# Kernel optimization log

Measured on AMD Instinct MI355X. Metric: run time of the kernel, lower is better.

Reference implementation:

```python
import jax, jax.numpy as jnp
import numpy as np


def setup_inputs() -> dict:
    key = jax.random.key(0)
    ks = jax.random.split(key, 5)
    B, T, I, H = 64, 512, 512, 512
    s_i = 1.0 / np.sqrt(H)
    return {
        "x": jax.random.normal(ks[0], (B, T, I), dtype=jnp.float32),
        "w_ih": jax.random.normal(ks[1], (4 * H, I), dtype=jnp.float32) * s_i,
        "w_hh": jax.random.normal(ks[2], (4 * H, H), dtype=jnp.float32) * s_i,
        "b_ih": jax.random.normal(ks[3], (4 * H,), dtype=jnp.float32) * s_i,
        "b_hh": jax.random.normal(ks[4], (4 * H,), dtype=jnp.float32) * s_i,
    }


def reference(x, w_ih, w_hh, b_ih, b_hh):
    # x: [B, T, I] (batch_first). Torch permutes to [T, B, I] then loops LSTMCell.
    B, T, I = x.shape
    H = w_hh.shape[1]
    # Precompute input contribution to gates for all timesteps: [T, B, 4H]
    x_gates = jnp.einsum('bti,gi->tbg', x, w_ih) + b_ih + b_hh
    h0 = jnp.zeros((B, H), dtype=x.dtype)  # hidden_init='zero'
    c0 = jnp.zeros((B, H), dtype=x.dtype)

    def step(carry, xg_t):
        h, c = carry
        gates = xg_t + h @ w_hh.T  # [B, 4H]
        i, f, g, o = jnp.split(gates, 4, axis=-1)  # torch LSTMCell order i,f,g,o
        i = jax.nn.sigmoid(i)
        f = jax.nn.sigmoid(f)
        g = jnp.tanh(g)
        o = jax.nn.sigmoid(o)
        c = f * c + i * g
        h = o * jnp.tanh(c)
        return (h, c), h

    (_, _), hs = jax.lax.scan(step, (h0, c0), x_gates)
    # return_sequences=True: torch stacks along dim 0 -> [T, B, H]
    return hs
```

## Files before the change

### kernel.cpp

```cpp
#include <hip/hip_runtime.h>
#include <stdint.h>


#define BATCH 64
#define TSTEPS 512
#define IDIM 512
#define HDIM 512
#define NGROUPS 8
#define BB 8
#define NWG (NGROUPS * 32)
#define HDAT_U64 (BB * (HDIM / 2))

typedef __attribute__((ext_vector_type(4))) float f32x4;
typedef __attribute__((ext_vector_type(8))) short bf16x8;
typedef __attribute__((ext_vector_type(4))) unsigned int u32x4;
typedef __attribute__((ext_vector_type(2))) unsigned int u32x2;

#define AS(p, v) __hip_atomic_store((p), (v), __ATOMIC_RELAXED, __HIP_MEMORY_SCOPE_AGENT)

__device__ inline unsigned short f2bf(float f) {
  unsigned u = __builtin_bit_cast(unsigned, f);
  u = (u + 0x7fffu + ((u >> 16) & 1u)) >> 16;
  return (unsigned short)u;
}
__device__ inline float fast_sigmoid(float x) { return 1.f / (1.f + __expf(-x)); }
__device__ inline float fast_tanh(float x) { return 1.f - 2.f / (__expf(2.f * x) + 1.f); }

__global__ void lstm_init(const float* __restrict__ b_ih, const float* __restrict__ b_hh,
                          float* __restrict__ bias, uint64_t* __restrict__ hdat) {
  const int i = blockIdx.x * blockDim.x + threadIdx.x;
  if (i < 4 * HDIM) bias[i] = b_ih[i] + b_hh[i];
  for (int j = i; j < 2 * NGROUPS * HDAT_U64; j += 2048) hdat[j] = 0ull;
}

__global__ __launch_bounds__(256, 1)
void lstm_persistent(const float* __restrict__ x,
                     const float* __restrict__ w_ih,
                     const float* __restrict__ w_hh,
                     const float* __restrict__ bias,
                     uint64_t* hdat,
                     float* __restrict__ out) {
  __shared__ unsigned short X_lds[2][8 * IDIM];
  __shared__ unsigned short H_lds[2][8 * HDIM];

  const int wg = blockIdx.x;
  const int group = wg >> 5;
  const int rank = wg & 31;
  const int b0 = group * BB;
  const int h0 = rank * 16;
  const int tid = threadIdx.x;
  const int wave = tid >> 6;
  const int lane = tid & 63;
  const int hi4 = lane >> 4;
  const int nn = lane & 15;

  const int growf = (nn & 3) * HDIM + h0 + wave * 4 + (nn >> 2);
  bf16x8 breg[32];
#pragma unroll
  for (int kt = 0; kt < 32; ++kt) {
    const int k = kt * 32 + hi4 * 8;
    const float* src = (k < IDIM) ? (w_ih + (size_t)growf * IDIM + k)
                                  : (w_hh + (size_t)growf * HDIM + (k - IDIM));
    bf16x8 v;
#pragma unroll
    for (int j = 0; j < 8; ++j) v[j] = (short)f2bf(src[j]);
    breg[kt] = v;
  }
  const int mycol = h0 + wave * 4 + hi4;
  const float bv0 = bias[0 * HDIM + mycol];
  const float bv1 = bias[1 * HDIM + mycol];
  const float bv2 = bias[2 * HDIM + mycol];
  const float bv3 = bias[3 * HDIM + mycol];

  const int bi = lane & 15;
  const int mr8 = bi & 7;
  const int rswz = mr8 << 4;

#pragma unroll
  for (int q = 0; q < 2; ++q) {
    const int r = wave + q * 4;
    const float* xp = x + ((size_t)(b0 + r) * TSTEPS + 0) * IDIM + lane * 8;
    float4 fa = *(const float4*)xp;
    float4 fb = *(const float4*)(xp + 4);
    bf16x8 v;
    v[0] = (short)f2bf(fa.x); v[1] = (short)f2bf(fa.y);
    v[2] = (short)f2bf(fa.z); v[3] = (short)f2bf(fa.w);
    v[4] = (short)f2bf(fb.x); v[5] = (short)f2bf(fb.y);
    v[6] = (short)f2bf(fb.z); v[7] = (short)f2bf(fb.w);
    *(bf16x8*)((char*)&X_lds[0][0] + ((r * 1024 + lane * 16) ^ ((r & 7) << 4))) = v;
  }
  float4 xfA[4], xfB[4];
#pragma unroll
  for (int q = 0; q < 2; ++q) {
    const float* xp = x + ((size_t)(b0 + wave + q * 4) * TSTEPS + 1) * IDIM + lane * 8;
    xfA[q * 2] = *(const float4*)xp;
    xfA[q * 2 + 1] = *(const float4*)(xp + 4);
  }
  __syncthreads();

  float c = 0.f;
  float hout[8];
  const size_t obase = (size_t)(b0 + bi) * HDIM + mycol;

  for (int tb = 0; tb < TSTEPS; tb += 8) {
#pragma unroll
    for (int u = 0; u < 8; ++u) {
      const int t = tb + u;
      const int cur = t & 1;
      const uint32_t tu = (uint32_t)t;

      f32x4 acc0 = {0.f, 0.f, 0.f, 0.f}, acc1 = {0.f, 0.f, 0.f, 0.f};
#pragma unroll
      for (int kt = 0; kt < 16; kt += 2) {
        bf16x8 a0 = *(const bf16x8*)((const char*)&X_lds[cur][0] +
                      ((mr8 * 1024 + (kt * 4 + hi4) * 16) ^ rswz));
        acc0 = __builtin_amdgcn_mfma_f32_16x16x32_bf16(breg[kt], a0, acc0, 0, 0, 0);
        bf16x8 a1 = *(const bf16x8*)((const char*)&X_lds[cur][0] +
                      ((mr8 * 1024 + ((kt + 1) * 4 + hi4) * 16) ^ rswz));
        acc1 = __builtin_amdgcn_mfma_f32_16x16x32_bf16(breg[kt + 1], a1, acc1, 0, 0, 0);
      }

      if (t > 0) {
        const uint64_t* dp = hdat + ((size_t)cur * NGROUPS + group) * HDAT_U64
                           + (size_t)wave * 512 + lane * 2;
        u32x4 d0, d1, d2, d3;
        while (true) {
          asm volatile(
            "global_load_dwordx4 %0, %4, off sc0 sc1\n\t"
            "global_load_dwordx4 %1, %4, off offset:1024 sc0 sc1\n\t"
            "global_load_dwordx4 %2, %4, off offset:2048 sc0 sc1\n\t"
            "global_load_dwordx4 %3, %4, off offset:3072 sc0 sc1\n\t"
            "s_waitcnt vmcnt(0)"
            : "=&v"(d0), "=&v"(d1), "=&v"(d2), "=&v"(d3)
            : "v"(dp) : "memory");
          __builtin_amdgcn_sched_barrier(0);
          bool ok = (d0[0] == tu) & (d0[2] == tu) & (d1[0] == tu) & (d1[2] == tu)
                  & (d2[0] == tu) & (d2[2] == tu) & (d3[0] == tu) & (d3[2] == tu);
          if (__all((int)ok)) break;
        }
#pragma unroll
        for (int j = 0; j < 4; ++j) {
          const int row = wave * 2 + (j >> 1);
          const int byte = (row * 1024 + (j & 1) * 512 + lane * 8) ^ ((row & 7) << 4);
          u32x2 w;
          if (j == 0)      { w[0] = d0[1]; w[1] = d0[3]; }
          else if (j == 1) { w[0] = d1[1]; w[1] = d1[3]; }
          else if (j == 2) { w[0] = d2[1]; w[1] = d2[3]; }
          else             { w[0] = d3[1]; w[1] = d3[3]; }
          *(u32x2*)((char*)&H_lds[cur][0] + byte) = w;
        }
      }

      if (t + 1 < TSTEPS) {
#pragma unroll
        for (int q = 0; q < 2; ++q) {
          float4 fa, fb;
          if ((u & 1) == 0) { fa = xfA[q * 2]; fb = xfA[q * 2 + 1]; }
          else              { fa = xfB[q * 2]; fb = xfB[q * 2 + 1]; }
          bf16x8 v;
          v[0] = (short)f2bf(fa.x); v[1] = (short)f2bf(fa.y);
          v[2] = (short)f2bf(fa.z); v[3] = (short)f2bf(fa.w);
          v[4] = (short)f2bf(fb.x); v[5] = (short)f2bf(fb.y);
          v[6] = (short)f2bf(fb.z); v[7] = (short)f2bf(fb.w);
          const int r = wave + q * 4;
          *(bf16x8*)((char*)&X_lds[cur ^ 1][0] + ((r * 1024 + lane * 16) ^ ((r & 7) << 4))) = v;
        }
      }
      __syncthreads();

      if (t + 2 < TSTEPS) {
#pragma unroll
        for (int q = 0; q < 2; ++q) {
          const float* xp = x + ((size_t)(b0 + wave + q * 4) * TSTEPS + (t + 2)) * IDIM + lane * 8;
          if ((u & 1) == 0) { xfB[q * 2] = *(const float4*)xp; xfB[q * 2 + 1] = *(const float4*)(xp + 4); }
          else              { xfA[q * 2] = *(const float4*)xp; xfA[q * 2 + 1] = *(const float4*)(xp + 4); }
        }
      }
      __builtin_amdgcn_sched_barrier(0);

      if (t > 0) {
#pragma unroll
        for (int kt = 0; kt < 16; kt += 2) {
          bf16x8 a0 = *(const bf16x8*)((const char*)&H_lds[cur][0] +
                        ((mr8 * 1024 + (kt * 4 + hi4) * 16) ^ rswz));
          acc0 = __builtin_amdgcn_mfma_f32_16x16x32_bf16(breg[16 + kt], a0, acc0, 0, 0, 0);
          bf16x8 a1 = *(const bf16x8*)((const char*)&H_lds[cur][0] +
                        ((mr8 * 1024 + ((kt + 1) * 4 + hi4) * 16) ^ rswz));
          acc1 = __builtin_amdgcn_mfma_f32_16x16x32_bf16(breg[17 + kt], a1, acc1, 0, 0, 0);
        }
      }

      const float gi = acc0[0] + acc1[0] + bv0;
      const float gf = acc0[1] + acc1[1] + bv1;
      const float gg = acc0[2] + acc1[2] + bv2;
      const float go = acc0[3] + acc1[3] + bv3;
      c = fast_sigmoid(gf) * c + fast_sigmoid(gi) * fast_tanh(gg);
      const float hval = fast_sigmoid(go) * fast_tanh(c);

      if (t + 1 < TSTEPS) {
        const unsigned hb = (unsigned)f2bf(hval);
        const unsigned pb = (unsigned)__shfl_xor((int)hb, 16, 64);
        if (bi < 8 && (hi4 & 1) == 0) {
          const uint64_t val = (uint64_t)(uint32_t)(t + 1)
                             | ((uint64_t)(hb | (pb << 16)) << 32);
          AS(hdat + ((size_t)((t + 1) & 1) * NGROUPS + group) * HDAT_U64
               + (size_t)bi * 256 + (mycol >> 1), val);
        }
      }
      hout[u] = hval;
    }
    if (bi < 8) {
#pragma unroll
      for (int k = 0; k < 8; ++k)
        out[(size_t)(tb + k) * (BATCH * HDIM) + obase] = hout[k];
    }
  }
}

extern "C" void kernel_launch(void* const* d_in, const int* in_sizes, int n_in,
                              void* d_out, int out_size, void* d_ws, size_t ws_size,
                              hipStream_t stream) {
  const float* x    = (const float*)d_in[0];
  const float* w_ih = (const float*)d_in[1];
  const float* w_hh = (const float*)d_in[2];
  const float* b_ih = (const float*)d_in[3];
  const float* b_hh = (const float*)d_in[4];
  float* out = (float*)d_out;

  char* ws = (char*)d_ws;
  float* bias = (float*)ws;
  uint64_t* hdat = (uint64_t*)(ws + 8192);

  lstm_init<<<8, 256, 0, stream>>>(b_ih, b_hh, bias, hdat);
  lstm_persistent<<<NWG, 256, 0, stream>>>(x, w_ih, w_hh, bias, hdat, out);
}
```

Baseline: 1.154 ms.

## Issue h-state flag loads early and overlap polling with input-projection MFMAs

```diff
diff --git a/kernel.cpp b/kernel.cpp
--- a/kernel.cpp
+++ b/kernel.cpp
@@ -13,9 +13,9 @@
 
 typedef __attribute__((ext_vector_type(4))) float f32x4;
 typedef __attribute__((ext_vector_type(8))) short bf16x8;
-typedef __attribute__((ext_vector_type(4))) unsigned int u32x4;
 typedef __attribute__((ext_vector_type(2))) unsigned int u32x2;
 
+#define AL(p) __hip_atomic_load((p), __ATOMIC_RELAXED, __HIP_MEMORY_SCOPE_AGENT)
 #define AS(p, v) __hip_atomic_store((p), (v), __ATOMIC_RELAXED, __HIP_MEMORY_SCOPE_AGENT)
 
 __device__ inline unsigned short f2bf(float f) {
@@ -23,8 +23,12 @@
   u = (u + 0x7fffu + ((u >> 16) & 1u)) >> 16;
   return (unsigned short)u;
 }
-__device__ inline float fast_sigmoid(float x) { return 1.f / (1.f + __expf(-x)); }
-__device__ inline float fast_tanh(float x) { return 1.f - 2.f / (__expf(2.f * x) + 1.f); }
+__device__ inline float fast_sigmoid(float x) {
+  return __builtin_amdgcn_rcpf(1.f + __expf(-x));
+}
+__device__ inline float fast_tanh(float x) {
+  return 1.f - 2.f * __builtin_amdgcn_rcpf(__expf(2.f * x) + 1.f);
+}
 
 __global__ void lstm_init(const float* __restrict__ b_ih, const float* __restrict__ b_hh,
                           float* __restrict__ bias, uint64_t* __restrict__ hdat) {
@@ -109,47 +113,16 @@
       const int cur = t & 1;
       const uint32_t tu = (uint32_t)t;
 
-      f32x4 acc0 = {0.f, 0.f, 0.f, 0.f}, acc1 = {0.f, 0.f, 0.f, 0.f};
-#pragma unroll
-      for (int kt = 0; kt < 16; kt += 2) {
-        bf16x8 a0 = *(const bf16x8*)((const char*)&X_lds[cur][0] +
-                      ((mr8 * 1024 + (kt * 4 + hi4) * 16) ^ rswz));
-        acc0 = __builtin_amdgcn_mfma_f32_16x16x32_bf16(breg[kt], a0, acc0, 0, 0, 0);
-        bf16x8 a1 = *(const bf16x8*)((const char*)&X_lds[cur][0] +
-                      ((mr8 * 1024 + ((kt + 1) * 4 + hi4) * 16) ^ rswz));
-        acc1 = __builtin_amdgcn_mfma_f32_16x16x32_bf16(breg[kt + 1], a1, acc1, 0, 0, 0);
-      }
-
+      const uint64_t* dp = hdat + ((size_t)cur * NGROUPS + group) * HDAT_U64
+                         + (size_t)wave * 512 + lane * 2;
+      uint64_t hu0, hu1, hu2, hu3, hu4, hu5, hu6, hu7;
       if (t > 0) {
-        const uint64_t* dp = hdat + ((size_t)cur * NGROUPS + group) * HDAT_U64
-                           + (size_t)wave * 512 + lane * 2;
-        u32x4 d0, d1, d2, d3;
-        while (true) {
-          asm volatile(
-            "global_load_dwordx4 %0, %4, off sc0 sc1\n\t"
-            "global_load_dwordx4 %1, %4, off offset:1024 sc0 sc1\n\t"
-            "global_load_dwordx4 %2, %4, off offset:2048 sc0 sc1\n\t"
-            "global_load_dwordx4 %3, %4, off offset:3072 sc0 sc1\n\t"
-            "s_waitcnt vmcnt(0)"
-            : "=&v"(d0), "=&v"(d1), "=&v"(d2), "=&v"(d3)
-            : "v"(dp) : "memory");
-          __builtin_amdgcn_sched_barrier(0);
-          bool ok = (d0[0] == tu) & (d0[2] == tu) & (d1[0] == tu) & (d1[2] == tu)
-                  & (d2[0] == tu) & (d2[2] == tu) & (d3[0] == tu) & (d3[2] == tu);
-          if (__all((int)ok)) break;
-        }
-#pragma unroll
-        for (int j = 0; j < 4; ++j) {
-          const int row = wave * 2 + (j >> 1);
-          const int byte = (row * 1024 + (j & 1) * 512 + lane * 8) ^ ((row & 7) << 4);
-          u32x2 w;
-          if (j == 0)      { w[0] = d0[1]; w[1] = d0[3]; }
-          else if (j == 1) { w[0] = d1[1]; w[1] = d1[3]; }
-          else if (j == 2) { w[0] = d2[1]; w[1] = d2[3]; }
-          else             { w[0] = d3[1]; w[1] = d3[3]; }
-          *(u32x2*)((char*)&H_lds[cur][0] + byte) = w;
-        }
-      }
+        hu0 = AL(dp);       hu1 = AL(dp + 1);
+        hu2 = AL(dp + 128); hu3 = AL(dp + 129);
+        hu4 = AL(dp + 256); hu5 = AL(dp + 257);
+        hu6 = AL(dp + 384); hu7 = AL(dp + 385);
+      }
+      __builtin_amdgcn_sched_barrier(0);
 
       if (t + 1 < TSTEPS) {
 #pragma unroll
@@ -166,6 +139,43 @@
           *(bf16x8*)((char*)&X_lds[cur ^ 1][0] + ((r * 1024 + lane * 16) ^ ((r & 7) << 4))) = v;
         }
       }
+
+      f32x4 acc0 = {0.f, 0.f, 0.f, 0.f}, acc1 = {0.f, 0.f, 0.f, 0.f};
+#pragma unroll
+      for (int kt = 0; kt < 16; kt += 2) {
+        bf16x8 a0 = *(const bf16x8*)((const char*)&X_lds[cur][0] +
+                      ((mr8 * 1024 + (kt * 4 + hi4) * 16) ^ rswz));
+        acc0 = __builtin_amdgcn_mfma_f32_16x16x32_bf16(breg[kt], a0, acc0, 0, 0, 0);
+        bf16x8 a1 = *(const bf16x8*)((const char*)&X_lds[cur][0] +
+                      ((mr8 * 1024 + ((kt + 1) * 4 + hi4) * 16) ^ rswz));
+        acc1 = __builtin_amdgcn_mfma_f32_16x16x32_bf16(breg[kt + 1], a1, acc1, 0, 0, 0);
+      }
+
+      if (t > 0) {
+        bool ok0 = false, ok1 = false, ok2 = false, ok3 = false;
+        while (true) {
+          if (!ok0) ok0 = __all((int)(((uint32_t)hu0 == tu) & ((uint32_t)hu1 == tu)));
+          if (!ok1) ok1 = __all((int)(((uint32_t)hu2 == tu) & ((uint32_t)hu3 == tu)));
+          if (!ok2) ok2 = __all((int)(((uint32_t)hu4 == tu) & ((uint32_t)hu5 == tu)));
+          if (!ok3) ok3 = __all((int)(((uint32_t)hu6 == tu) & ((uint32_t)hu7 == tu)));
+          if (ok0 & ok1 & ok2 & ok3) break;
+          if (!ok0) { hu0 = AL(dp);       hu1 = AL(dp + 1); }
+          if (!ok1) { hu2 = AL(dp + 128); hu3 = AL(dp + 129); }
+          if (!ok2) { hu4 = AL(dp + 256); hu5 = AL(dp + 257); }
+          if (!ok3) { hu6 = AL(dp + 384); hu7 = AL(dp + 385); }
+        }
+        {
+          const int r0 = wave * 2;
+          u32x2 w0 = { (uint32_t)(hu0 >> 32), (uint32_t)(hu1 >> 32) };
+          u32x2 w1 = { (uint32_t)(hu2 >> 32), (uint32_t)(hu3 >> 32) };
+          u32x2 w2 = { (uint32_t)(hu4 >> 32), (uint32_t)(hu5 >> 32) };
+          u32x2 w3 = { (uint32_t)(hu6 >> 32), (uint32_t)(hu7 >> 32) };
+          *(u32x2*)((char*)&H_lds[cur][0] + ((r0 * 1024 + lane * 8) ^ ((r0 & 7) << 4))) = w0;
+          *(u32x2*)((char*)&H_lds[cur][0] + ((r0 * 1024 + 512 + lane * 8) ^ ((r0 & 7) << 4))) = w1;
+          *(u32x2*)((char*)&H_lds[cur][0] + (((r0 + 1) * 1024 + lane * 8) ^ (((r0 + 1) & 7) << 4))) = w2;
+          *(u32x2*)((char*)&H_lds[cur][0] + (((r0 + 1) * 1024 + 512 + lane * 8) ^ (((r0 + 1) & 7) << 4))) = w3;
+        }
+      }
       __syncthreads();
 
       if (t + 2 < TSTEPS) {
```

Measured after the change: 2.401 ms. 108% more time.

## Interleave two independent batch chains per workgroup to hide recurrence latency

Applied to the files above, without the earlier changes.

```diff
diff --git a/kernel.cpp b/kernel.cpp
--- a/kernel.cpp
+++ b/kernel.cpp
@@ -6,9 +6,9 @@
 #define TSTEPS 512
 #define IDIM 512
 #define HDIM 512
-#define NGROUPS 8
+#define NCH 8
 #define BB 8
-#define NWG (NGROUPS * 32)
+#define NWG 128
 #define HDAT_U64 (BB * (HDIM / 2))
 
 typedef __attribute__((ext_vector_type(4))) float f32x4;
@@ -23,14 +23,18 @@
   u = (u + 0x7fffu + ((u >> 16) & 1u)) >> 16;
   return (unsigned short)u;
 }
-__device__ inline float fast_sigmoid(float x) { return 1.f / (1.f + __expf(-x)); }
-__device__ inline float fast_tanh(float x) { return 1.f - 2.f / (__expf(2.f * x) + 1.f); }
+__device__ inline float fast_sigmoid(float x) {
+  return __builtin_amdgcn_rcpf(1.f + __expf(-x));
+}
+__device__ inline float fast_tanh(float x) {
+  return 1.f - 2.f * __builtin_amdgcn_rcpf(__expf(2.f * x) + 1.f);
+}
 
 __global__ void lstm_init(const float* __restrict__ b_ih, const float* __restrict__ b_hh,
                           float* __restrict__ bias, uint64_t* __restrict__ hdat) {
   const int i = blockIdx.x * blockDim.x + threadIdx.x;
   if (i < 4 * HDIM) bias[i] = b_ih[i] + b_hh[i];
-  for (int j = i; j < 2 * NGROUPS * HDAT_U64; j += 2048) hdat[j] = 0ull;
+  for (int j = i; j < 2 * NCH * HDAT_U64; j += 2048) hdat[j] = 0ull;
 }
 
 __global__ __launch_bounds__(256, 1)
@@ -40,13 +44,18 @@
                      const float* __restrict__ bias,
                      uint64_t* hdat,
                      float* __restrict__ out) {
-  __shared__ unsigned short X_lds[2][8 * IDIM];
-  __shared__ unsigned short H_lds[2][8 * HDIM];
+  __shared__ unsigned short XA_lds[2][8 * IDIM];
+  __shared__ unsigned short HA_lds[2][8 * HDIM];
+  __shared__ unsigned short XB_lds[2][8 * IDIM];
+  __shared__ unsigned short HB_lds[2][8 * HDIM];
 
   const int wg = blockIdx.x;
-  const int group = wg >> 5;
+  const int pair = wg >> 5;
   const int rank = wg & 31;
-  const int b0 = group * BB;
+  const int chA = pair * 2;
+  const int chB = pair * 2 + 1;
+  const int b0A = chA * BB;
+  const int b0B = chB * BB;
   const int h0 = rank * 16;
   const int tid = threadIdx.x;
   const int wave = tid >> 6;
@@ -76,145 +85,158 @@
   const int mr8 = bi & 7;
   const int rswz = mr8 << 4;
 
+#define STAGE_X(XL, buf, fa, fb, r)                                          \
+  {                                                                          \
+    bf16x8 v_;                                                               \
+    v_[0] = (short)f2bf(fa.x); v_[1] = (short)f2bf(fa.y);                    \
+    v_[2] = (short)f2bf(fa.z); v_[3] = (short)f2bf(fa.w);                    \
+    v_[4] = (short)f2bf(fb.x); v_[5] = (short)f2bf(fb.y);                    \
+    v_[6] = (short)f2bf(fb.z); v_[7] = (short)f2bf(fb.w);                    \
+    *(bf16x8*)((char*)&XL[buf][0] + (((r) * 1024 + lane * 16) ^ (((r) & 7) << 4))) = v_; \
+  }
+
 #pragma unroll
   for (int q = 0; q < 2; ++q) {
     const int r = wave + q * 4;
-    const float* xp = x + ((size_t)(b0 + r) * TSTEPS + 0) * IDIM + lane * 8;
-    float4 fa = *(const float4*)xp;
-    float4 fb = *(const float4*)(xp + 4);
-    bf16x8 v;
-    v[0] = (short)f2bf(fa.x); v[1] = (short)f2bf(fa.y);
-    v[2] = (short)f2bf(fa.z); v[3] = (short)f2bf(fa.w);
-    v[4] = (short)f2bf(fb.x); v[5] = (short)f2bf(fb.y);
-    v[6] = (short)f2bf(fb.z); v[7] = (short)f2bf(fb.w);
-    *(bf16x8*)((char*)&X_lds[0][0] + ((r * 1024 + lane * 16) ^ ((r & 7) << 4))) = v;
-  }
-  float4 xfA[4], xfB[4];
+    const float* xpA = x + ((size_t)(b0A + r) * TSTEPS + 0) * IDIM + lane * 8;
+    float4 fa = *(const float4*)xpA, fb = *(const float4*)(xpA + 4);
+    STAGE_X(XA_lds, 0, fa, fb, r)
+    const float* xpB = x + ((size_t)(b0B + r) * TSTEPS + 0) * IDIM + lane * 8;
+    fa = *(const float4*)xpB; fb = *(const float4*)(xpB + 4);
+    STAGE_X(XB_lds, 0, fa, fb, r)
+  }
+  float4 xfPA[4], xfQA[4], xfPB[4], xfQB[4];
 #pragma unroll
   for (int q = 0; q < 2; ++q) {
-    const float* xp = x + ((size_t)(b0 + wave + q * 4) * TSTEPS + 1) * IDIM + lane * 8;
-    xfA[q * 2] = *(const float4*)xp;
-    xfA[q * 2 + 1] = *(const float4*)(xp + 4);
+    const float* xpA = x + ((size_t)(b0A + wave + q * 4) * TSTEPS + 1) * IDIM + lane * 8;
+    xfPA[q * 2] = *(const float4*)xpA; xfPA[q * 2 + 1] = *(const float4*)(xpA + 4);
+    const float* xpB = x + ((size_t)(b0B + wave + q * 4) * TSTEPS + 1) * IDIM + lane * 8;
+    xfPB[q * 2] = *(const float4*)xpB; xfPB[q * 2 + 1] = *(const float4*)(xpB + 4);
   }
   __syncthreads();
 
-  float c = 0.f;
-  float hout[8];
-  const size_t obase = (size_t)(b0 + bi) * HDIM + mycol;
-
-  for (int tb = 0; tb < TSTEPS; tb += 8) {
-#pragma unroll
-    for (int u = 0; u < 8; ++u) {
+  float cA = 0.f, cB = 0.f;
+  float houtA[4], houtB[4];
+  const size_t obaseA = (size_t)(b0A + bi) * HDIM + mycol;
+  const size_t obaseB = (size_t)(b0B + bi) * HDIM + mycol;
+
+#define CHAIN_STEP(XL, HL, cc, xfP, xfQ, chid, b0c, houtc)                   \
+  {                                                                          \
+    const int cur = t & 1;                                                   \
+                                                  \
+    f32x4 acc0 = {0.f, 0.f, 0.f, 0.f}, acc1 = {0.f, 0.f, 0.f, 0.f};          \
+    _Pragma("unroll")                                                        \
+    for (int kt = 0; kt < 16; kt += 2) {                                     \
+      bf16x8 a0 = *(const bf16x8*)((const char*)&XL[cur][0] +                \
+                    ((mr8 * 1024 + (kt * 4 + hi4) * 16) ^ rswz));            \
+      acc0 = __builtin_amdgcn_mfma_f32_16x16x32_bf16(breg[kt], a0, acc0, 0, 0, 0); \
+      bf16x8 a1 = *(const bf16x8*)((const char*)&XL[cur][0] +                \
+                    ((mr8 * 1024 + ((kt + 1) * 4 + hi4) * 16) ^ rswz));      \
+      acc1 = __builtin_amdgcn_mfma_f32_16x16x32_bf16(breg[kt + 1], a1, acc1, 0, 0, 0); \
+    }                                                                        \
+                                                          \
+    if (t + 1 < TSTEPS) {                                                    \
+      _Pragma("unroll")                                                      \
+      for (int q = 0; q < 2; ++q) {                                          \
+        float4 fa, fb;                                                       \
+        if ((u & 1) == 0) { fa = xfP[q * 2]; fb = xfP[q * 2 + 1]; }          \
+        else              { fa = xfQ[q * 2]; fb = xfQ[q * 2 + 1]; }          \
+        const int r = wave + q * 4;                                          \
+        STAGE_X(XL, cur ^ 1, fa, fb, r)                                      \
+      }                                                                      \
+    }                                                                        \
+                                                  \
+    if (t > 0) {                                                             \
+      const uint64_t* dp = hdat + ((size_t)cur * NCH + (chid)) * HDAT_U64    \
+                         + (size_t)wave * 512 + lane * 2;                    \
+      u32x4 d0, d1, d2, d3;                                                  \
+      const uint32_t tu = (uint32_t)t;                                       \
+      while (true) {                                                         \
+        asm volatile(                                                        \
+          "global_load_dwordx4 %0, %4, off sc0 sc1\n\t"                      \
+          "global_load_dwordx4 %1, %4, off offset:1024 sc0 sc1\n\t"          \
+          "global_load_dwordx4 %2, %4, off offset:2048 sc0 sc1\n\t"          \
+          "global_load_dwordx4 %3, %4, off offset:3072 sc0 sc1\n\t"          \
+          "s_waitcnt vmcnt(0)"                                               \
+          : "=&v"(d0), "=&v"(d1), "=&v"(d2), "=&v"(d3)                       \
+          : "v"(dp) : "memory");                                             \
+        __builtin_amdgcn_sched_barrier(0);                                   \
+        bool ok = (d0[0] == tu) & (d0[2] == tu) & (d1[0] == tu) & (d1[2] == tu) \
+                & (d2[0] == tu) & (d2[2] == tu) & (d3[0] == tu) & (d3[2] == tu); \
+        if (__all((int)ok)) break;                                           \
+      }                                                                      \
+      _Pragma("unroll")                                                      \
+      for (int j = 0; j < 4; ++j) {                                          \
+        const int row = wave * 2 + (j >> 1);                                 \
+        const int byte = (row * 1024 + (j & 1) * 512 + lane * 8) ^ ((row & 7) << 4); \
+        u32x2 w;                                                             \
+        if (j == 0)      { w[0] = d0[1]; w[1] = d0[3]; }                     \
+        else if (j == 1) { w[0] = d1[1]; w[1] = d1[3]; }                     \
+        else if (j == 2) { w[0] = d2[1]; w[1] = d2[3]; }                     \
+        else             { w[0] = d3[1]; w[1] = d3[3]; }                     \
+        *(u32x2*)((char*)&HL[cur][0] + byte) = w;                            \
+      }                                                                      \
+    }                                                                        \
+    __syncthreads();                         \
+                                          \
+    if (t + 2 < TSTEPS) {                                                    \
+      _Pragma("unroll")                                                      \
+      for (int q = 0; q < 2; ++q) {                                          \
+        const float* xp = x + ((size_t)((b0c) + wave + q * 4) * TSTEPS + (t + 2)) * IDIM + lane * 8; \
+        if ((u & 1) == 0) { xfQ[q * 2] = *(const float4*)xp; xfQ[q * 2 + 1] = *(const float4*)(xp + 4); } \
+        else              { xfP[q * 2] = *(const float4*)xp; xfP[q * 2 + 1] = *(const float4*)(xp + 4); } \
+      }                                                                      \
+    }                                                                        \
+    __builtin_amdgcn_sched_barrier(0);                                       \
+                                                  \
+    if (t > 0) {                                                             \
+      _Pragma("unroll")                                                      \
+      for (int kt = 0; kt < 16; kt += 2) {                                   \
+        bf16x8 a0 = *(const bf16x8*)((const char*)&HL[cur][0] +              \
+                      ((mr8 * 1024 + (kt * 4 + hi4) * 16) ^ rswz));          \
+        acc0 = __builtin_amdgcn_mfma_f32_16x16x32_bf16(breg[16 + kt], a0, acc0, 0, 0, 0); \
+        bf16x8 a1 = *(const bf16x8*)((const char*)&HL[cur][0] +              \
+                      ((mr8 * 1024 + ((kt + 1) * 4 + hi4) * 16) ^ rswz));    \
+        acc1 = __builtin_amdgcn_mfma_f32_16x16x32_bf16(breg[17 + kt], a1, acc1, 0, 0, 0); \
+      }                                                                      \
+    }                                                                        \
+                                                  \
+    const float gi = acc0[0] + acc1[0] + bv0;                                \
+    const float gf = acc0[1] + acc1[1] + bv1;                                \
+    const float gg = acc0[2] + acc1[2] + bv2;                                \
+    const float go = acc0[3] + acc1[3] + bv3;                                \
+    cc = fast_sigmoid(gf) * cc + fast_sigmoid(gi) * fast_tanh(gg);           \
+    const float hval = fast_sigmoid(go) * fast_tanh(cc);                     \
+    if (t + 1 < TSTEPS) {                                                    \
+      const unsigned hb = (unsigned)f2bf(hval);                              \
+      const unsigned pb = (unsigned)__shfl_xor((int)hb, 16, 64);             \
+      if (bi < 8 && (hi4 & 1) == 0) {                                        \
+        const uint64_t val = (uint64_t)(uint32_t)(t + 1)                     \
+                           | ((uint64_t)(hb | (pb << 16)) << 32);            \
+        AS(hdat + ((size_t)((t + 1) & 1) * NCH + (chid)) * HDAT_U64          \
+             + (size_t)bi * 256 + (mycol >> 1), val);                        \
+      }                                                                      \
+    }                                                                        \
+    houtc[u] = hval;                                                         \
+  }
+
+  for (int tb = 0; tb < TSTEPS; tb += 4) {
+#pragma unroll
+    for (int u = 0; u < 4; ++u) {
       const int t = tb + u;
-      const int cur = t & 1;
-      const uint32_t tu = (uint32_t)t;
-
-      f32x4 acc0 = {0.f, 0.f, 0.f, 0.f}, acc1 = {0.f, 0.f, 0.f, 0.f};
-#pragma unroll
-      for (int kt = 0; kt < 16; kt += 2) {
-        bf16x8 a0 = *(const bf16x8*)((const char*)&X_lds[cur][0] +
-                      ((mr8 * 1024 + (kt * 4 + hi4) * 16) ^ rswz));
-        acc0 = __builtin_amdgcn_mfma_f32_16x16x32_bf16(breg[kt], a0, acc0, 0, 0, 0);
-        bf16x8 a1 = *(const bf16x8*)((const char*)&X_lds[cur][0] +
-                      ((mr8 * 1024 + ((kt + 1) * 4 + hi4) * 16) ^ rswz));
-        acc1 = __builtin_amdgcn_mfma_f32_16x16x32_bf16(breg[kt + 1], a1, acc1, 0, 0, 0);
-      }
-
-      if (t > 0) {
-        const uint64_t* dp = hdat + ((size_t)cur * NGROUPS + group) * HDAT_U64
-                           + (size_t)wave * 512 + lane * 2;
-        u32x4 d0, d1, d2, d3;
-        while (true) {
-          asm volatile(
-            "global_load_dwordx4 %0, %4, off sc0 sc1\n\t"
-            "global_load_dwordx4 %1, %4, off offset:1024 sc0 sc1\n\t"
-            "global_load_dwordx4 %2, %4, off offset:2048 sc0 sc1\n\t"
-            "global_load_dwordx4 %3, %4, off offset:3072 sc0 sc1\n\t"
-            "s_waitcnt vmcnt(0)"
-            : "=&v"(d0), "=&v"(d1), "=&v"(d2), "=&v"(d3)
-            : "v"(dp) : "memory");
-          __builtin_amdgcn_sched_barrier(0);
-          bool ok = (d0[0] == tu) & (d0[2] == tu) & (d1[0] == tu) & (d1[2] == tu)
-                  & (d2[0] == tu) & (d2[2] == tu) & (d3[0] == tu) & (d3[2] == tu);
-          if (__all((int)ok)) break;
-        }
-#pragma unroll
-        for (int j = 0; j < 4; ++j) {
-          const int row = wave * 2 + (j >> 1);
-          const int byte = (row * 1024 + (j & 1) * 512 + lane * 8) ^ ((row & 7) << 4);
-          u32x2 w;
-          if (j == 0)      { w[0] = d0[1]; w[1] = d0[3]; }
-          else if (j == 1) { w[0] = d1[1]; w[1] = d1[3]; }
-          else if (j == 2) { w[0] = d2[1]; w[1] = d2[3]; }
-          else             { w[0] = d3[1]; w[1] = d3[3]; }
-          *(u32x2*)((char*)&H_lds[cur][0] + byte) = w;
-        }
-      }
-
-      if (t + 1 < TSTEPS) {
-#pragma unroll
-        for (int q = 0; q < 2; ++q) {
-          float4 fa, fb;
-          if ((u & 1) == 0) { fa = xfA[q * 2]; fb = xfA[q * 2 + 1]; }
-          else              { fa = xfB[q * 2]; fb = xfB[q * 2 + 1]; }
-          bf16x8 v;
-          v[0] = (short)f2bf(fa.x); v[1] = (short)f2bf(fa.y);
-          v[2] = (short)f2bf(fa.z); v[3] = (short)f2bf(fa.w);
-          v[4] = (short)f2bf(fb.x); v[5] = (short)f2bf(fb.y);
-          v[6] = (short)f2bf(fb.z); v[7] = (short)f2bf(fb.w);
-          const int r = wave + q * 4;
-          *(bf16x8*)((char*)&X_lds[cur ^ 1][0] + ((r * 1024 + lane * 16) ^ ((r & 7) << 4))) = v;
-        }
-      }
-      __syncthreads();
-
-      if (t + 2 < TSTEPS) {
-#pragma unroll
-        for (int q = 0; q < 2; ++q) {
-          const float* xp = x + ((size_t)(b0 + wave + q * 4) * TSTEPS + (t + 2)) * IDIM + lane * 8;
-          if ((u & 1) == 0) { xfB[q * 2] = *(const float4*)xp; xfB[q * 2 + 1] = *(const float4*)(xp + 4); }
-          else              { xfA[q * 2] = *(const float4*)xp; xfA[q * 2 + 1] = *(const float4*)(xp + 4); }
-        }
-      }
-      __builtin_amdgcn_sched_barrier(0);
-
-      if (t > 0) {
-#pragma unroll
-        for (int kt = 0; kt < 16; kt += 2) {
-          bf16x8 a0 = *(const bf16x8*)((const char*)&H_lds[cur][0] +
-                        ((mr8 * 1024 + (kt * 4 + hi4) * 16) ^ rswz));
-          acc0 = __builtin_amdgcn_mfma_f32_16x16x32_bf16(breg[16 + kt], a0, acc0, 0, 0, 0);
-          bf16x8 a1 = *(const bf16x8*)((const char*)&H_lds[cur][0] +
-                        ((mr8 * 1024 + ((kt + 1) * 4 + hi4) * 16) ^ rswz));
-          acc1 = __builtin_amdgcn_mfma_f32_16x16x32_bf16(breg[17 + kt], a1, acc1, 0, 0, 0);
-        }
-      }
-
-      const float gi = acc0[0] + acc1[0] + bv0;
-      const float gf = acc0[1] + acc1[1] + bv1;
-      const float gg = acc0[2] + acc1[2] + bv2;
-      const float go = acc0[3] + acc1[3] + bv3;
-      c = fast_sigmoid(gf) * c + fast_sigmoid(gi) * fast_tanh(gg);
-      const float hval = fast_sigmoid(go) * fast_tanh(c);
-
-      if (t + 1 < TSTEPS) {
-        const unsigned hb = (unsigned)f2bf(hval);
-        const unsigned pb = (unsigned)__shfl_xor((int)hb, 16, 64);
-        if (bi < 8 && (hi4 & 1) == 0) {
-          const uint64_t val = (uint64_t)(uint32_t)(t + 1)
-                             | ((uint64_t)(hb | (pb << 16)) << 32);
-          AS(hdat + ((size_t)((t + 1) & 1) * NGROUPS + group) * HDAT_U64
-               + (size_t)bi * 256 + (mycol >> 1), val);
-        }
-      }
-      hout[u] = hval;
+      CHAIN_STEP(XA_lds, HA_lds, cA, xfPA, xfQA, chA, b0A, houtA)
+      CHAIN_STEP(XB_lds, HB_lds, cB, xfPB, xfQB, chB, b0B, houtB)
     }
     if (bi < 8) {
 #pragma unroll
-      for (int k = 0; k < 8; ++k)
-        out[(size_t)(tb + k) * (BATCH * HDIM) + obase] = hout[k];
+      for (int k = 0; k < 4; ++k) {
+        out[(size_t)(tb + k) * (BATCH * HDIM) + obaseA] = houtA[k];
+        out[(size_t)(tb + k) * (BATCH * HDIM) + obaseB] = houtB[k];
+      }
     }
   }
+#undef CHAIN_STEP
+#undef STAGE_X
 }
 
 extern "C" void kernel_launch(void* const* d_in, const int* in_sizes, int n_in,
```

After: 1.698 ms. 1.47x slower.
